# Kernel optimization log

Measured on AMD Instinct MI355X. Metric: run time of the kernel, lower is better.

## Reference

```python
import jax, jax.numpy as jnp
import numpy as np

B, T, D = 2, 2048, 1024
H = 16
HD = D // H
NE = 17  # n_edge_types + 1

def setup_inputs() -> dict:
    key = jax.random.key(0)
    ks = jax.random.split(key, 6)
    x = jax.random.normal(ks[0], (B, T, D), dtype=jnp.float32)
    graph_adj = jax.random.uniform(ks[1], (B, T, T), dtype=jnp.float32)
    edge_types = jax.random.randint(ks[2], (B, T, T), 0, NE, dtype=jnp.int32)
    Wqkv = jax.random.normal(ks[3], (D, 3 * D), dtype=jnp.float32) * (D ** -0.5)
    Wproj = jax.random.normal(ks[4], (D, D), dtype=jnp.float32) * (D ** -0.5)
    adj_bias = jnp.zeros((H,), dtype=jnp.float32)
    edge_table = jax.random.normal(ks[5], (NE, H), dtype=jnp.float32) * 0.02
    return {"x": x, "graph_adj": graph_adj, "edge_types": edge_types,
            "Wqkv": Wqkv, "Wproj": Wproj, "adj_bias": adj_bias,
            "edge_table": edge_table}

def reference(x, graph_adj, edge_types, Wqkv, Wproj, adj_bias, edge_table):
    Bc, Tc, C = x.shape
    qkv = (x @ Wqkv).reshape(Bc, Tc, 3, H, HD)
    q, k, v = qkv[:, :, 0], qkv[:, :, 1], qkv[:, :, 2]  # [B,T,H,HD]
    scale = 1.0 / jnp.sqrt(jnp.asarray(HD, dtype=x.dtype))
    # scores: [B,H,T,T]
    attn = jnp.einsum('bqhd,bkhd->bhqk', q, k) * scale
    # adjacency bias per head
    attn = attn + adj_bias[None, :, None, None] * graph_adj[:, None, :, :]
    # edge-type bias: lookup [B,T,T,H] -> [B,H,T,T]
    etype_b = edge_table[edge_types]  # [B,T,T,H]
    attn = attn + jnp.transpose(etype_b, (0, 3, 1, 2))
    # causal mask (upper triangle, diag=1)
    causal = jnp.triu(jnp.ones((Tc, Tc), dtype=bool), k=1)
    attn = jnp.where(causal[None, None, :, :], jnp.asarray(-jnp.inf, dtype=attn.dtype), attn)
    attn = jax.nn.softmax(attn, axis=-1)
    out = jnp.einsum('bhqk,bkhd->bqhd', attn, v).reshape(Bc, Tc, C)
    return out @ Wproj
```

## Files before the change

### kernel.cpp

```cpp
#include <hip/hip_runtime.h>
#include <stdint.h>

#define TT 2048
#define HH 16
#define LOG2E 1.44269504089f

typedef _Float16 f16;
typedef __attribute__((ext_vector_type(8))) _Float16 f16x8;
typedef __attribute__((ext_vector_type(4))) float f32x4;
typedef unsigned short ushort_t;

__device__ __forceinline__ void gl_lds16(const void* g, void* l){
  __builtin_amdgcn_global_load_lds(
      (__attribute__((address_space(1))) void*)(void*)g,
      (__attribute__((address_space(3))) void*)l, 16, 0, 0);
}

__device__ __forceinline__ void lds_barrier(){
  __asm__ volatile("s_waitcnt lgkmcnt(0)\n\ts_barrier" ::: "memory");
}

template<int CTRL>
__device__ __forceinline__ float dpp_mov(float x){
  int xi = __builtin_bit_cast(int, x);
  return __builtin_bit_cast(float,
      __builtin_amdgcn_update_dpp(xi, xi, CTRL, 0xF, 0xF, false));
}
__device__ __forceinline__ float row_red_max(float x){
  x = fmaxf(x, dpp_mov<0xB1>(x));
  x = fmaxf(x, dpp_mov<0x4E>(x));
  x = fmaxf(x, dpp_mov<0x124>(x));
  x = fmaxf(x, dpp_mov<0x128>(x));
  return x;
}
__device__ __forceinline__ float row_red_sum(float x){
  x += dpp_mov<0xB1>(x);
  x += dpp_mov<0x4E>(x);
  x += dpp_mov<0x124>(x);
  x += dpp_mov<0x128>(x);
  return x;
}

struct SchedT { unsigned short v[80]; };
static constexpr SchedT make_sched(){
  SchedT s{};
  int idx = 0;
  for (int size = 8; size >= 1; --size){
    for (int qt = 31; qt >= 8; --qt){
      int full = qt >> 3;
      int tail = (qt & 7) + 1;
      if (size == 8)
        for (int ci = 0; ci < full; ++ci)
          s.v[idx++] = (unsigned short)(qt | (ci << 8));
      if (tail == size)
        s.v[idx++] = (unsigned short)(qt | (full << 8));
    }
    s.v[idx++] = (unsigned short)(size - 1);
  }
  return s;
}
__constant__ SchedT SCHED = make_sched();

__device__ __forceinline__ int slot_base(int qt){
  return (qt < 16) ? 2 * (qt - 8)
       : (qt < 24) ? 16 + 3 * (qt - 16)
                   : 40 + 4 * (qt - 24);
}

__global__ __launch_bounds__(256) void cvt_f2h_kernel(const float4* __restrict__ in,
                                                      uint2* __restrict__ out, int n4){
  int i = blockIdx.x * 256 + threadIdx.x;
  if (i >= n4) return;
  float4 v = in[i];
  union { f16 h[4]; uint2 u; } o;
  o.h[0] = (f16)v.x; o.h[1] = (f16)v.y; o.h[2] = (f16)v.z; o.h[3] = (f16)v.w;
  out[i] = o.u;
}

__global__ __launch_bounds__(256) void pack_bias_kernel(const float* __restrict__ gadj,
                                                        const int* __restrict__ etype,
                                                        uint32_t* __restrict__ out){
  int bid = blockIdx.x;
  int b = bid / 528, ti = bid - b * 528;
  int qt = (int)((sqrtf(8.f * (float)ti + 1.f) - 1.f) * 0.5f);
  while ((qt + 1) * (qt + 2) / 2 <= ti) ++qt;
  while (qt * (qt + 1) / 2 > ti) --qt;
  int kt = ti - qt * (qt + 1) / 2;

  int t = threadIdx.x;
  int row = t >> 2, c0 = (t & 3) << 4;
  size_t src = ((size_t)b * TT + qt * 64 + row) * TT + kt * 64 + c0;
  uint32_t* dst = out + (size_t)bid * 4096;
  int wq = (row >> 4) * 64 + ((row & 15) >> 2) * 16;
  int jbase = (t & 3) * 4 + (row & 3);
  #pragma unroll
  for (int v4 = 0; v4 < 4; ++v4){
    float4 g = *(const float4*)(gadj + src + v4 * 4);
    int4   e = *(const int4*)(etype + src + v4 * 4);
    union { f16 h; ushort_t u; } c;
    c.h = (f16)g.x; dst[(wq + v4 * 4 + 0) * 16 + jbase] = (uint32_t)c.u | ((uint32_t)e.x << 16);
    c.h = (f16)g.y; dst[(wq + v4 * 4 + 1) * 16 + jbase] = (uint32_t)c.u | ((uint32_t)e.y << 16);
    c.h = (f16)g.z; dst[(wq + v4 * 4 + 2) * 16 + jbase] = (uint32_t)c.u | ((uint32_t)e.z << 16);
    c.h = (f16)g.w; dst[(wq + v4 * 4 + 3) * 16 + jbase] = (uint32_t)c.u | ((uint32_t)e.w << 16);
  }
}

__global__ __launch_bounds__(256) void transpose_cvt_kernel(const float* __restrict__ in,
                                                            f16* __restrict__ out, int R, int C){
  __shared__ float tile[64][65];
  int c0 = blockIdx.x * 64, r0 = blockIdx.y * 64;
  int t = threadIdx.x;
  int row = t >> 2, cs = (t & 3) << 4;
  const float4* src = (const float4*)(in + (size_t)(r0 + row) * C + c0 + cs);
  float4 a = src[0], b = src[1], c = src[2], d = src[3];
  float* tr = &tile[row][cs];
  tr[0]=a.x; tr[1]=a.y; tr[2]=a.z;  tr[3]=a.w;
  tr[4]=b.x; tr[5]=b.y; tr[6]=b.z;  tr[7]=b.w;
  tr[8]=c.x; tr[9]=c.y; tr[10]=c.z; tr[11]=c.w;
  tr[12]=d.x;tr[13]=d.y;tr[14]=d.z; tr[15]=d.w;
  __syncthreads();
  f16 tmp[16];
  #pragma unroll
  for (int j = 0; j < 16; ++j) tmp[j] = (f16)tile[cs + j][row];
  f16* dst = out + (size_t)(c0 + row) * R + r0 + cs;
  *(uint4*)dst = *(uint4*)&tmp[0];
  *(uint4*)(dst + 8) = *(uint4*)&tmp[8];
}

__global__ __launch_bounds__(256) void gemm_f16_kernel(const f16* __restrict__ A,
                                                       const f16* __restrict__ Bt,
                                                       void* __restrict__ Cout,
                                                       int M, int N, int K, int out_f32){
  __shared__ __align__(16) f16 As[128 * 32];
  __shared__ __align__(16) f16 Bs[128 * 32];
  int t = threadIdx.x;
  int w = t >> 6, lane = t & 63;
  int wm = (w >> 1) * 64, wn = (w & 1) * 64;
  int lrow = lane & 15, quad = lane >> 4;
  int bm = blockIdx.y, bn = blockIdx.x;

  f32x4 acc[4][4];
  for (int i = 0; i < 4; ++i)
    for (int j = 0; j < 4; ++j)
      for (int r = 0; r < 4; ++r) acc[i][j][r] = 0.f;

  const int nk = K >> 5;
  for (int kt = 0; kt < nk; ++kt){
    int k0 = kt << 5;
    __syncthreads();
    #pragma unroll
    for (int i = 0; i < 2; ++i){
      int c = (w << 7) + (i << 6) + lane;
      gl_lds16(A  + (size_t)((bm << 7) + (c >> 2)) * K + k0 + ((c & 3) << 3),
               As + ((w << 7) + (i << 6)) * 8);
      gl_lds16(Bt + (size_t)((bn << 7) + (c >> 2)) * K + k0 + ((c & 3) << 3),
               Bs + ((w << 7) + (i << 6)) * 8);
    }
    __syncthreads();
    f16x8 af[4], bfr[4];
    #pragma unroll
    for (int mi = 0; mi < 4; ++mi)
      af[mi] = *(const f16x8*)(As + (wm + mi * 16 + lrow) * 32 + quad * 8);
    #pragma unroll
    for (int ni = 0; ni < 4; ++ni)
      bfr[ni] = *(const f16x8*)(Bs + (wn + ni * 16 + lrow) * 32 + quad * 8);
    #pragma unroll
    for (int mi = 0; mi < 4; ++mi)
      #pragma unroll
      for (int ni = 0; ni < 4; ++ni)
        acc[mi][ni] = __builtin_amdgcn_mfma_f32_16x16x32_f16(af[mi], bfr[ni], acc[mi][ni], 0, 0, 0);
  }

  #pragma unroll
  for (int mi = 0; mi < 4; ++mi)
    #pragma unroll
    for (int ni = 0; ni < 4; ++ni)
      #pragma unroll
      for (int r = 0; r < 4; ++r){
        int row = (bm << 7) + wm + mi * 16 + quad * 4 + r;
        int col = (bn << 7) + wn + ni * 16 + lrow;
        float val = acc[mi][ni][r];
        if (out_f32) ((float*)Cout)[(size_t)row * N + col] = val;
        else         ((f16*)Cout)[(size_t)row * N + col] = (f16)val;
      }
}

__global__ __launch_bounds__(256, 4) void attn_kernel(const f16* __restrict__ qkv,
                                                      const uint32_t* __restrict__ pbias,
                                                      const float* __restrict__ adj_bias,
                                                      const float* __restrict__ edge_table,
                                                      f16* __restrict__ attn_out,
                                                      f16* __restrict__ Opart,
                                                      float* __restrict__ MLpart){
  __shared__ __align__(16) f16 Ks[64 * 72];
  __shared__ __align__(16) f16 Vt[64 * 72];
  __shared__ __align__(16) f16 Ps[4][16 * 72];
  __shared__ float edge_lds[32 * 17];

  int bx = blockIdx.x;
  int bh = bx & 31;
  int h = bh & 15, b = bh >> 4;
  int ej = SCHED.v[bx >> 5];
  int qt = ej & 31, ci = ej >> 8;
  int ksrt = ci << 3;
  int kend = min(qt, ksrt + 7);
  bool whole = (qt < 8);

  int t = threadIdx.x;
  int w = t >> 6, lane = t & 63;
  int lrow = lane & 15, quad = lane >> 4;

  for (int i = t; i < 544; i += 256)
    edge_lds[i] = edge_table[(i % 17) * HH + h] * LOG2E;
  float adjb = adj_bias[h] * LOG2E;
  int erep = (lane & 31) * 17;

  int q0 = qt * 64 + w * 16;
  const size_t qrow = ((size_t)b * TT + q0 + lrow) * 3072 + h * 64;
  f16x8 qf0 = *(const f16x8*)(qkv + qrow + quad * 8);
  f16x8 qf1 = *(const f16x8*)(qkv + qrow + 32 + quad * 8);

  f32x4 o[4];
  for (int i = 0; i < 4; ++i)
    for (int r = 0; r < 4; ++r) o[i][r] = 0.f;
  float mrun[4] = {-1e30f, -1e30f, -1e30f, -1e30f};
  float lrun[4] = {0.f, 0.f, 0.f, 0.f};

  const int keyA = (t >> 3) << 1;
  const int hdA  = (t & 7) << 3;
  const int sA   = ((keyA >> 3) ^ (hdA >> 3)) & 7;
  const f16* kbase = qkv + (size_t)b * TT * 3072 + 1024 + h * 64;
  const f16* vbase = qkv + (size_t)b * TT * 3072 + 2048 + h * 64;
  const size_t koffA = (size_t)keyA * 3072 + hdA;
  const size_t koffB = koffA + 3072;

  const float SCL = 0.125f * LOG2E;

  const int tribase = b * 528 + ((qt * (qt + 1)) >> 1);
  const uint32_t* bthread = pbias + ((size_t)t << 4);
  const int qgb = q0 + quad * 4;

  uint4 ka, kb, va, vb;
  {
    const f16* kr = kbase + (size_t)(ksrt * 64) * 3072;
    const f16* vr = vbase + (size_t)(ksrt * 64) * 3072;
    ka = *(const uint4*)(kr + koffA); kb = *(const uint4*)(kr + koffB);
    va = *(const uint4*)(vr + koffA); vb = *(const uint4*)(vr + koffB);
  }

  for (int kt2 = ksrt; kt2 <= kend; ++kt2){
    lds_barrier();
    union B4 { uint4 v; uint32_t e[4]; } bb0, bb1, bb2, bb3;
    {
      const uint32_t* tp = bthread + ((size_t)(tribase + kt2) << 12);
      bb0.v = *(const uint4*)(tp + 0);
      bb1.v = *(const uint4*)(tp + 4);
      bb2.v = *(const uint4*)(tp + 8);
      bb3.v = *(const uint4*)(tp + 12);
    }
    *(uint4*)(Ks + keyA * 72 + hdA) = ka;
    *(uint4*)(Ks + (keyA + 1) * 72 + hdA) = kb;
    {
      union { uint4 u; f16 hh[8]; } ua, ub;
      ua.u = va; ub.u = vb;
      #pragma unroll
      for (int jj = 0; jj < 8; ++jj){
        union { f16 h[2]; uint32_t wv; } pr;
        pr.h[0] = ua.hh[jj]; pr.h[1] = ub.hh[jj];
        *(uint32_t*)(Vt + (hdA + jj) * 72 + (sA << 3) + (keyA & 7)) = pr.wv;
      }
    }
    if (kt2 < kend){
      const f16* kr = kbase + (size_t)((kt2 + 1) * 64) * 3072;
      const f16* vr = vbase + (size_t)((kt2 + 1) * 64) * 3072;
      ka = *(const uint4*)(kr + koffA); kb = *(const uint4*)(kr + koffB);
      va = *(const uint4*)(vr + koffA); vb = *(const uint4*)(vr + koffB);
    }
    lds_barrier();

    f32x4 sf[4];
    #pragma unroll
    for (int nb = 0; nb < 4; ++nb){
      f32x4 s = {0.f, 0.f, 0.f, 0.f};
      f16x8 kf0 = *(const f16x8*)(Ks + (nb * 16 + lrow) * 72 + quad * 8);
      f16x8 kf1 = *(const f16x8*)(Ks + (nb * 16 + lrow) * 72 + 32 + quad * 8);
      s = __builtin_amdgcn_mfma_f32_16x16x32_f16(qf0, kf0, s, 0, 0, 0);
      s = __builtin_amdgcn_mfma_f32_16x16x32_f16(qf1, kf1, s, 0, 0, 0);
      sf[nb] = s;
    }

    int kgb = kt2 * 64 + lrow;
    float sarr[4][4];
    bool diag = (kt2 == qt);
#define MASK_NB(nb, BB)                                                          \
    {                                                                            \
      int kg = kgb + nb * 16;                                                    \
      _Pragma("unroll")                                                          \
      for (int r = 0; r < 4; ++r){                                               \
        float v;                                                                 \
        if (diag && kg > qgb + r) v = -1e30f;                                    \
        else {                                                                   \
          uint32_t bp = BB.e[r];                                                 \
          union { ushort_t u; f16 h; } cv; cv.u = (ushort_t)bp;                  \
          v = sf[nb][r] * SCL + adjb * (float)cv.h + edge_lds[erep + (bp >> 16)];\
        }                                                                        \
        sarr[nb][r] = v;                                                         \
      }                                                                          \
    }
    MASK_NB(0, bb0)
    MASK_NB(1, bb1)
    MASK_NB(2, bb2)
    MASK_NB(3, bb3)
#undef MASK_NB

    float mx[4];
    bool need = false;
    #pragma unroll
    for (int r = 0; r < 4; ++r){
      float m_ = fmaxf(fmaxf(sarr[0][r], sarr[1][r]), fmaxf(sarr[2][r], sarr[3][r]));
      m_ = row_red_max(m_);
      mx[r] = m_;
      need = need || (m_ > mrun[r] + 5.0f);
    }
    if (__any(need)){
      #pragma unroll
      for (int r = 0; r < 4; ++r){
        float mnew = fmaxf(mrun[r], mx[r]);
        float alpha = exp2f(mrun[r] - mnew);
        lrun[r] *= alpha;
        #pragma unroll
        for (int nbh = 0; nbh < 4; ++nbh) o[nbh][r] *= alpha;
        mrun[r] = mnew;
      }
    }
    float pv_[4][4];
    #pragma unroll
    for (int r = 0; r < 4; ++r){
      float rs = 0.f;
      #pragma unroll
      for (int nb = 0; nb < 4; ++nb){
        float p = exp2f(sarr[nb][r] - mrun[r]);
        pv_[nb][r] = p; rs += p;
      }
      rs = row_red_sum(rs);
      lrun[r] += rs;
    }

    f16* Pw = &Ps[w][0];
    #pragma unroll
    for (int nb = 0; nb < 4; ++nb)
      #pragma unroll
      for (int r = 0; r < 4; ++r)
        Pw[(quad * 4 + r) * 72 + nb * 16 + lrow] = (f16)pv_[nb][r];
    __asm__ volatile("s_waitcnt lgkmcnt(0)" ::: "memory");

    #pragma unroll
    for (int cc = 0; cc < 2; ++cc){
      f16x8 pf = *(const f16x8*)(Pw + lrow * 72 + cc * 32 + quad * 8);
      #pragma unroll
      for (int nbh = 0; nbh < 4; ++nbh){
        int hd = nbh * 16 + lrow;
        int sb = (hd >> 3) & 7;
        f16x8 vf = *(const f16x8*)(Vt + hd * 72 + (((cc * 4 + quad) ^ sb) << 3));
        o[nbh] = __builtin_amdgcn_mfma_f32_16x16x32_f16(pf, vf, o[nbh], 0, 0, 0);
      }
    }
  }

  if (whole){
    float inv[4];
    #pragma unroll
    for (int r = 0; r < 4; ++r) inv[r] = 1.0f / lrun[r];
    #pragma unroll
    for (int nbh = 0; nbh < 4; ++nbh)
      #pragma unroll
      for (int r = 0; r < 4; ++r){
        int qg = q0 + quad * 4 + r;
        int col = h * 64 + nbh * 16 + lrow;
        attn_out[((size_t)b * TT + qg) * 1024 + col] = (f16)(o[nbh][r] * inv[r]);
      }
  } else {
    int slot = bh * 72 + slot_base(qt) + ci;
    f16* Ob = Opart + (size_t)slot * 4096;
    #pragma unroll
    for (int nbh = 0; nbh < 4; ++nbh)
      #pragma unroll
      for (int r = 0; r < 4; ++r)
        Ob[(w * 16 + quad * 4 + r) * 64 + nbh * 16 + lrow] = (f16)o[nbh][r];
    if (lrow == 0){
      #pragma unroll
      for (int r = 0; r < 4; ++r){
        int qq = w * 16 + quad * 4 + r;
        MLpart[(size_t)slot * 128 + qq] = mrun[r];
        MLpart[(size_t)slot * 128 + 64 + qq] = lrun[r];
      }
    }
  }
}

__global__ __launch_bounds__(256) void combine_kernel(const f16* __restrict__ Opart,
                                                      const float* __restrict__ ML,
                                                      f16* __restrict__ attn_out){
  int qt = blockIdx.x + 8;
  int bh = blockIdx.y;
  int nch = (qt >> 3) + 1;
  int slot0 = bh * 72 + slot_base(qt);
  int t = threadIdx.x;
  int q = t >> 2;
  int hd0 = (t & 3) << 4;

  float m[4], l[4];
  float M = -1e30f;
  #pragma unroll
  for (int c = 0; c < 4; ++c){
    if (c < nch){
      m[c] = ML[(size_t)(slot0 + c) * 128 + q];
      l[c] = ML[(size_t)(slot0 + c) * 128 + 64 + q];
      M = fmaxf(M, m[c]);
    } else { m[c] = -1e30f; l[c] = 0.f; }
  }
  float acc[16];
  #pragma unroll
  for (int i = 0; i < 16; ++i) acc[i] = 0.f;
  float L = 0.f;
  #pragma unroll
  for (int c = 0; c < 4; ++c){
    if (c < nch){
      float wgt = exp2f(m[c] - M);
      L += l[c] * wgt;
      const f16* O = Opart + (size_t)(slot0 + c) * 4096 + q * 64 + hd0;
      f16x8 a0 = *(const f16x8*)O, a1 = *(const f16x8*)(O + 8);
      #pragma unroll
      for (int i = 0; i < 8; ++i){
        acc[i]     += (float)a0[i] * wgt;
        acc[i + 8] += (float)a1[i] * wgt;
      }
    }
  }
  float invL = 1.0f / L;
  f16 outv[16];
  #pragma unroll
  for (int i = 0; i < 16; ++i) outv[i] = (f16)(acc[i] * invL);
  int b = bh >> 4, h = bh & 15;
  f16* dst = attn_out + ((size_t)b * TT + qt * 64 + q) * 1024 + h * 64 + hd0;
  *(uint4*)dst = *(uint4*)&outv[0];
  *(uint4*)(dst + 8) = *(uint4*)&outv[8];
}

extern "C" void kernel_launch(void* const* d_in, const int* in_sizes, int n_in,
                              void* d_out, int out_size, void* d_ws, size_t ws_size,
                              hipStream_t stream){
  (void)in_sizes; (void)n_in; (void)out_size; (void)ws_size;
  const float* x_f32  = (const float*)d_in[0];
  const float* gadj   = (const float*)d_in[1];
  const int*   etype  = (const int*)d_in[2];
  const float* wqkv   = (const float*)d_in[3];
  const float* wproj  = (const float*)d_in[4];
  const float* adjb   = (const float*)d_in[5];
  const float* etab   = (const float*)d_in[6];

  char* ws = (char*)d_ws;
  f16*     x_f16  = (f16*)(ws);
  f16*     qkv    = (f16*)(ws + (8u  << 20));
  f16*     wqkvT  = (f16*)(ws + (32u << 20));
  f16*     Opart  = (f16*)(ws + (32u << 20));
  f16*     wprojT = (f16*)(ws + (51u << 20));
  float*   MLpart = (float*)(ws + (53u << 20));
  uint32_t* pbias = (uint32_t*)(ws + (55u << 20));
  f16*     attn_o = x_f16;

  cvt_f2h_kernel<<<4096, 256, 0, stream>>>((const float4*)x_f32, (uint2*)x_f16, 1048576);
  pack_bias_kernel<<<1056, 256, 0, stream>>>(gadj, etype, pbias);
  transpose_cvt_kernel<<<dim3(48, 16), 256, 0, stream>>>(wqkv, wqkvT, 1024, 3072);
  transpose_cvt_kernel<<<dim3(16, 16), 256, 0, stream>>>(wproj, wprojT, 1024, 1024);
  gemm_f16_kernel<<<dim3(24, 32), 256, 0, stream>>>(x_f16, wqkvT, qkv, 4096, 3072, 1024, 0);
  attn_kernel<<<2560, 256, 0, stream>>>(qkv, pbias, adjb, etab, attn_o, Opart, MLpart);
  combine_kernel<<<dim3(24, 32), 256, 0, stream>>>(Opart, MLpart, attn_o);
  gemm_f16_kernel<<<dim3(8, 32), 256, 0, stream>>>(attn_o, wprojT, d_out, 4096, 1024, 1024, 1);
}
```

Before: 282.9 us.

## Process two query tiles per attention block to reuse loaded K/V tiles

```diff
diff --git a/kernel.cpp b/kernel.cpp
--- a/kernel.cpp
+++ b/kernel.cpp
@@ -41,30 +41,25 @@
   return x;
 }
 
-struct SchedT { unsigned short v[80]; };
+struct SchedT { unsigned short v[40]; };
 static constexpr SchedT make_sched(){
-  SchedT s{};
-  int idx = 0;
-  for (int size = 8; size >= 1; --size){
-    for (int qt = 31; qt >= 8; --qt){
-      int full = qt >> 3;
-      int tail = (qt & 7) + 1;
+  SchedT s{}; int idx = 0;
+  for (int size = 8; size >= 1; --size)
+    for (int J = 15; J >= 0; --J){
+      int NT = 2 * J + 2;
+      int f = NT >> 3, tail = NT - (f << 3);
       if (size == 8)
-        for (int ci = 0; ci < full; ++ci)
-          s.v[idx++] = (unsigned short)(qt | (ci << 8));
-      if (tail == size)
-        s.v[idx++] = (unsigned short)(qt | (full << 8));
-    }
-    s.v[idx++] = (unsigned short)(size - 1);
-  }
+        for (int ci = 0; ci < f; ++ci) s.v[idx++] = (unsigned short)(J | (ci << 4));
+      if (tail == size) s.v[idx++] = (unsigned short)(J | (f << 4));
+    }
   return s;
 }
 __constant__ SchedT SCHED = make_sched();
 
-__device__ __forceinline__ int slot_base(int qt){
-  return (qt < 16) ? 2 * (qt - 8)
-       : (qt < 24) ? 16 + 3 * (qt - 16)
-                   : 40 + 4 * (qt - 24);
+__device__ __forceinline__ int slot_base(int J){
+  return (J < 8) ? 2 * (J - 4)
+       : (J < 12) ? 8 + 3 * (J - 8)
+                  : 20 + 4 * (J - 12);
 }
 
 __global__ __launch_bounds__(256) void cvt_f2h_kernel(const float4* __restrict__ in,
@@ -185,7 +180,7 @@
       }
 }
 
-__global__ __launch_bounds__(256, 4) void attn_kernel(const f16* __restrict__ qkv,
+__global__ __launch_bounds__(256, 3) void attn_kernel(const f16* __restrict__ qkv,
                                                       const uint32_t* __restrict__ pbias,
                                                       const float* __restrict__ adj_bias,
                                                       const float* __restrict__ edge_table,
@@ -194,17 +189,18 @@
                                                       float* __restrict__ MLpart){
   __shared__ __align__(16) f16 Ks[64 * 72];
   __shared__ __align__(16) f16 Vt[64 * 72];
-  __shared__ __align__(16) f16 Ps[4][16 * 72];
+  __shared__ __align__(16) f16 Ps[4][2][16 * 72];
   __shared__ float edge_lds[32 * 17];
 
   int bx = blockIdx.x;
   int bh = bx & 31;
   int h = bh & 15, b = bh >> 4;
-  int ej = SCHED.v[bx >> 5];
-  int qt = ej & 31, ci = ej >> 8;
-  int ksrt = ci << 3;
-  int kend = min(qt, ksrt + 7);
-  bool whole = (qt < 8);
+  int e = SCHED.v[bx >> 5];
+  int J = e & 15, ci = e >> 4;
+  int kts = ci << 3;
+  int kte = min(2 * J + 1, kts + 7);
+  bool whole = (J <= 3);
+  int qtA = 2 * J, qtB = 2 * J + 1;
 
   int t = threadIdx.x;
   int w = t >> 6, lane = t & 63;
@@ -215,16 +211,20 @@
   float adjb = adj_bias[h] * LOG2E;
   int erep = (lane & 31) * 17;
 
-  int q0 = qt * 64 + w * 16;
-  const size_t qrow = ((size_t)b * TT + q0 + lrow) * 3072 + h * 64;
-  f16x8 qf0 = *(const f16x8*)(qkv + qrow + quad * 8);
-  f16x8 qf1 = *(const f16x8*)(qkv + qrow + 32 + quad * 8);
-
-  f32x4 o[4];
+  int qa0 = J * 128 + w * 16;
+  int qb0 = qa0 + 64;
+  const size_t qrowA = ((size_t)b * TT + qa0 + lrow) * 3072 + h * 64;
+  const size_t qrowB = ((size_t)b * TT + qb0 + lrow) * 3072 + h * 64;
+  f16x8 qfa0 = *(const f16x8*)(qkv + qrowA + quad * 8);
+  f16x8 qfa1 = *(const f16x8*)(qkv + qrowA + 32 + quad * 8);
+  f16x8 qfb0 = *(const f16x8*)(qkv + qrowB + quad * 8);
+  f16x8 qfb1 = *(const f16x8*)(qkv + qrowB + 32 + quad * 8);
+
+  f32x4 oa[4], ob[4];
   for (int i = 0; i < 4; ++i)
-    for (int r = 0; r < 4; ++r) o[i][r] = 0.f;
-  float mrun[4] = {-1e30f, -1e30f, -1e30f, -1e30f};
-  float lrun[4] = {0.f, 0.f, 0.f, 0.f};
+    for (int r = 0; r < 4; ++r){ oa[i][r] = 0.f; ob[i][r] = 0.f; }
+  float mra[4] = {-1e30f,-1e30f,-1e30f,-1e30f}, mrb[4] = {-1e30f,-1e30f,-1e30f,-1e30f};
+  float lra[4] = {0.f,0.f,0.f,0.f},             lrb[4] = {0.f,0.f,0.f,0.f};
 
   const int keyA = (t >> 3) << 1;
   const int hdA  = (t & 7) << 3;
@@ -236,27 +236,33 @@
 
   const float SCL = 0.125f * LOG2E;
 
-  const int tribase = b * 528 + ((qt * (qt + 1)) >> 1);
-  const uint32_t* bthread = pbias + ((size_t)t << 4);
-  const int qgb = q0 + quad * 4;
+  const int triA = b * 528 + ((qtA * (qtA + 1)) >> 1);
+  const int triB = b * 528 + ((qtB * (qtB + 1)) >> 1);
+  const uint32_t* bthr = pbias + ((size_t)t << 4);
+  const int qgbA = qa0 + quad * 4;
+  const int qgbB = qb0 + quad * 4;
 
   uint4 ka, kb, va, vb;
   {
-    const f16* kr = kbase + (size_t)(ksrt * 64) * 3072;
-    const f16* vr = vbase + (size_t)(ksrt * 64) * 3072;
+    const f16* kr = kbase + (size_t)(kts * 64) * 3072;
+    const f16* vr = vbase + (size_t)(kts * 64) * 3072;
     ka = *(const uint4*)(kr + koffA); kb = *(const uint4*)(kr + koffB);
     va = *(const uint4*)(vr + koffA); vb = *(const uint4*)(vr + koffB);
   }
 
-  for (int kt2 = ksrt; kt2 <= kend; ++kt2){
+  for (int kt2 = kts; kt2 <= kte; ++kt2){
+    bool act_a = (kt2 <= qtA);
     lds_barrier();
-    union B4 { uint4 v; uint32_t e[4]; } bb0, bb1, bb2, bb3;
+    union B4 { uint4 v; uint32_t e[4]; } a0, a1, a2, a3, c0, c1, c2, c3;
+    if (act_a){
+      const uint32_t* tp = bthr + ((size_t)(triA + kt2) << 12);
+      a0.v = *(const uint4*)(tp + 0);  a1.v = *(const uint4*)(tp + 4);
+      a2.v = *(const uint4*)(tp + 8);  a3.v = *(const uint4*)(tp + 12);
+    }
     {
-      const uint32_t* tp = bthread + ((size_t)(tribase + kt2) << 12);
-      bb0.v = *(const uint4*)(tp + 0);
-      bb1.v = *(const uint4*)(tp + 4);
-      bb2.v = *(const uint4*)(tp + 8);
-      bb3.v = *(const uint4*)(tp + 12);
+      const uint32_t* tp = bthr + ((size_t)(triB + kt2) << 12);
+      c0.v = *(const uint4*)(tp + 0);  c1.v = *(const uint4*)(tp + 4);
+      c2.v = *(const uint4*)(tp + 8);  c3.v = *(const uint4*)(tp + 12);
     }
     *(uint4*)(Ks + keyA * 72 + hdA) = ka;
     *(uint4*)(Ks + (keyA + 1) * 72 + hdA) = kb;
@@ -270,7 +276,7 @@
         *(uint32_t*)(Vt + (hdA + jj) * 72 + (sA << 3) + (keyA & 7)) = pr.wv;
       }
     }
-    if (kt2 < kend){
+    if (kt2 < kte){
       const f16* kr = kbase + (size_t)((kt2 + 1) * 64) * 3072;
       const f16* vr = vbase + (size_t)((kt2 + 1) * 64) * 3072;
       ka = *(const uint4*)(kr + koffA); kb = *(const uint4*)(kr + koffB);
@@ -278,121 +284,161 @@
     }
     lds_barrier();
 
-    f32x4 sf[4];
+    f32x4 sa[4], sbv[4];
     #pragma unroll
     for (int nb = 0; nb < 4; ++nb){
-      f32x4 s = {0.f, 0.f, 0.f, 0.f};
       f16x8 kf0 = *(const f16x8*)(Ks + (nb * 16 + lrow) * 72 + quad * 8);
       f16x8 kf1 = *(const f16x8*)(Ks + (nb * 16 + lrow) * 72 + 32 + quad * 8);
-      s = __builtin_amdgcn_mfma_f32_16x16x32_f16(qf0, kf0, s, 0, 0, 0);
-      s = __builtin_amdgcn_mfma_f32_16x16x32_f16(qf1, kf1, s, 0, 0, 0);
-      sf[nb] = s;
+      f32x4 s = {0.f, 0.f, 0.f, 0.f};
+      if (act_a){
+        s = __builtin_amdgcn_mfma_f32_16x16x32_f16(qfa0, kf0, s, 0, 0, 0);
+        s = __builtin_amdgcn_mfma_f32_16x16x32_f16(qfa1, kf1, s, 0, 0, 0);
+      }
+      sa[nb] = s;
+      f32x4 s2 = {0.f, 0.f, 0.f, 0.f};
+      s2 = __builtin_amdgcn_mfma_f32_16x16x32_f16(qfb0, kf0, s2, 0, 0, 0);
+      s2 = __builtin_amdgcn_mfma_f32_16x16x32_f16(qfb1, kf1, s2, 0, 0, 0);
+      sbv[nb] = s2;
     }
 
     int kgb = kt2 * 64 + lrow;
-    float sarr[4][4];
-    bool diag = (kt2 == qt);
-#define MASK_NB(nb, BB)                                                          \
+
+#define MASK_NB(SARR, SF, nb, BB, DIAG, QGB)                                     \
     {                                                                            \
       int kg = kgb + nb * 16;                                                    \
       _Pragma("unroll")                                                          \
       for (int r = 0; r < 4; ++r){                                               \
         float v;                                                                 \
-        if (diag && kg > qgb + r) v = -1e30f;                                    \
+        if (DIAG && kg > QGB + r) v = -1e30f;                                    \
         else {                                                                   \
           uint32_t bp = BB.e[r];                                                 \
           union { ushort_t u; f16 h; } cv; cv.u = (ushort_t)bp;                  \
-          v = sf[nb][r] * SCL + adjb * (float)cv.h + edge_lds[erep + (bp >> 16)];\
+          v = SF[nb][r] * SCL + adjb * (float)cv.h + edge_lds[erep + (bp >> 16)];\
         }                                                                        \
-        sarr[nb][r] = v;                                                         \
+        SARR[nb][r] = v;                                                         \
       }                                                                          \
     }
-    MASK_NB(0, bb0)
-    MASK_NB(1, bb1)
-    MASK_NB(2, bb2)
-    MASK_NB(3, bb3)
+
+#define SOFTMAX_SUB(SARR, MR, LR, OO, PV)                                        \
+    {                                                                            \
+      float mx[4]; bool need = false;                                            \
+      _Pragma("unroll")                                                          \
+      for (int r = 0; r < 4; ++r){                                               \
+        float m_ = fmaxf(fmaxf(SARR[0][r], SARR[1][r]),                          \
+                         fmaxf(SARR[2][r], SARR[3][r]));                         \
+        m_ = row_red_max(m_);                                                    \
+        mx[r] = m_;                                                              \
+        need = need || (m_ > MR[r] + 5.0f);                                      \
+      }                                                                          \
+      if (__any(need)){                                                          \
+        _Pragma("unroll")                                                        \
+        for (int r = 0; r < 4; ++r){                                             \
+          float mnew = fmaxf(MR[r], mx[r]);                                      \
+          float alpha = exp2f(MR[r] - mnew);                                     \
+          LR[r] *= alpha;                                                        \
+          _Pragma("unroll")                                                      \
+          for (int nbh = 0; nbh < 4; ++nbh) OO[nbh][r] *= alpha;                 \
+          MR[r] = mnew;                                                          \
+        }                                                                        \
+      }                                                                          \
+      _Pragma("unroll")                                                          \
+      for (int r = 0; r < 4; ++r){                                               \
+        float rs = 0.f;                                                          \
+        _Pragma("unroll")                                                        \
+        for (int nb = 0; nb < 4; ++nb){                                          \
+          float p = exp2f(SARR[nb][r] - MR[r]);                                  \
+          PV[nb][r] = p; rs += p;                                                \
+        }                                                                        \
+        rs = row_red_sum(rs);                                                    \
+        LR[r] += rs;                                                             \
+      }                                                                          \
+    }
+
+    float pva[4][4], pvb[4][4];
+    if (act_a){
+      bool diagA = (kt2 == qtA);
+      float sarr[4][4];
+      MASK_NB(sarr, sa, 0, a0, diagA, qgbA)
+      MASK_NB(sarr, sa, 1, a1, diagA, qgbA)
+      MASK_NB(sarr, sa, 2, a2, diagA, qgbA)
+      MASK_NB(sarr, sa, 3, a3, diagA, qgbA)
+      SOFTMAX_SUB(sarr, mra, lra, oa, pva)
+      f16* Pw = &Ps[w][0][0];
+      #pragma unroll
+      for (int nb = 0; nb < 4; ++nb)
+        #pragma unroll
+        for (int r = 0; r < 4; ++r)
+          Pw[(quad * 4 + r) * 72 + nb * 16 + lrow] = (f16)pva[nb][r];
+    }
+    {
+      bool diagB = (kt2 == qtB);
+      float sarr[4][4];
+      MASK_NB(sarr, sbv, 0, c0, diagB, qgbB)
+      MASK_NB(sarr, sbv, 1, c1, diagB, qgbB)
+      MASK_NB(sarr, sbv, 2, c2, diagB, qgbB)
+      MASK_NB(sarr, sbv, 3, c3, diagB, qgbB)
+      SOFTMAX_SUB(sarr, mrb, lrb, ob, pvb)
+      f16* Pw = &Ps[w][1][0];
+      #pragma unroll
+      for (int nb = 0; nb < 4; ++nb)
+        #pragma unroll
+        for (int r = 0; r < 4; ++r)
+          Pw[(quad * 4 + r) * 72 + nb * 16 + lrow] = (f16)pvb[nb][r];
+    }
 #undef MASK_NB
-
-    float mx[4];
-    bool need = false;
-    #pragma unroll
-    for (int r = 0; r < 4; ++r){
-      float m_ = fmaxf(fmaxf(sarr[0][r], sarr[1][r]), fmaxf(sarr[2][r], sarr[3][r]));
-      m_ = row_red_max(m_);
-      mx[r] = m_;
-      need = need || (m_ > mrun[r] + 5.0f);
-    }
-    if (__any(need)){
-      #pragma unroll
-      for (int r = 0; r < 4; ++r){
-        float mnew = fmaxf(mrun[r], mx[r]);
-        float alpha = exp2f(mrun[r] - mnew);
-        lrun[r] *= alpha;
-        #pragma unroll
-        for (int nbh = 0; nbh < 4; ++nbh) o[nbh][r] *= alpha;
-        mrun[r] = mnew;
-      }
-    }
-    float pv_[4][4];
-    #pragma unroll
-    for (int r = 0; r < 4; ++r){
-      float rs = 0.f;
-      #pragma unroll
-      for (int nb = 0; nb < 4; ++nb){
-        float p = exp2f(sarr[nb][r] - mrun[r]);
-        pv_[nb][r] = p; rs += p;
-      }
-      rs = row_red_sum(rs);
-      lrun[r] += rs;
-    }
-
-    f16* Pw = &Ps[w][0];
-    #pragma unroll
-    for (int nb = 0; nb < 4; ++nb)
-      #pragma unroll
-      for (int r = 0; r < 4; ++r)
-        Pw[(quad * 4 + r) * 72 + nb * 16 + lrow] = (f16)pv_[nb][r];
+#undef SOFTMAX_SUB
     __asm__ volatile("s_waitcnt lgkmcnt(0)" ::: "memory");
 
     #pragma unroll
     for (int cc = 0; cc < 2; ++cc){
-      f16x8 pf = *(const f16x8*)(Pw + lrow * 72 + cc * 32 + quad * 8);
+      f16x8 pfa = {};
+      if (act_a) pfa = *(const f16x8*)(&Ps[w][0][0] + lrow * 72 + cc * 32 + quad * 8);
+      f16x8 pfb = *(const f16x8*)(&Ps[w][1][0] + lrow * 72 + cc * 32 + quad * 8);
       #pragma unroll
       for (int nbh = 0; nbh < 4; ++nbh){
         int hd = nbh * 16 + lrow;
         int sb = (hd >> 3) & 7;
         f16x8 vf = *(const f16x8*)(Vt + hd * 72 + (((cc * 4 + quad) ^ sb) << 3));
-        o[nbh] = __builtin_amdgcn_mfma_f32_16x16x32_f16(pf, vf, o[nbh], 0, 0, 0);
+        if (act_a) oa[nbh] = __builtin_amdgcn_mfma_f32_16x16x32_f16(pfa, vf, oa[nbh], 0, 0, 0);
+        ob[nbh] = __builtin_amdgcn_mfma_f32_16x16x32_f16(pfb, vf, ob[nbh], 0, 0, 0);
       }
     }
   }
 
   if (whole){
-    float inv[4];
-    #pragma unroll
-    for (int r = 0; r < 4; ++r) inv[r] = 1.0f / lrun[r];
+    float inva[4], invb[4];
+    #pragma unroll
+    for (int r = 0; r < 4; ++r){ inva[r] = 1.0f / lra[r]; invb[r] = 1.0f / lrb[r]; }
     #pragma unroll
     for (int nbh = 0; nbh < 4; ++nbh)
       #pragma unroll
       for (int r = 0; r < 4; ++r){
-        int qg = q0 + quad * 4 + r;
         int col = h * 64 + nbh * 16 + lrow;
-        attn_out[((size_t)b * TT + qg) * 1024 + col] = (f16)(o[nbh][r] * inv[r]);
+        int qga = qa0 + quad * 4 + r;
+        attn_out[((size_t)b * TT + qga) * 1024 + col] = (f16)(oa[nbh][r] * inva[r]);
+        int qgb2 = qb0 + quad * 4 + r;
+        attn_out[((size_t)b * TT + qgb2) * 1024 + col] = (f16)(ob[nbh][r] * invb[r]);
       }
   } else {
-    int slot = bh * 72 + slot_base(qt) + ci;
-    f16* Ob = Opart + (size_t)slot * 4096;
+    int slot = bh * 36 + slot_base(J) + ci;
+    f16* Ob = Opart + (size_t)slot * 8192;
     #pragma unroll
     for (int nbh = 0; nbh < 4; ++nbh)
       #pragma unroll
-      for (int r = 0; r < 4; ++r)
-        Ob[(w * 16 + quad * 4 + r) * 64 + nbh * 16 + lrow] = (f16)o[nbh][r];
+      for (int r = 0; r < 4; ++r){
+        int col = nbh * 16 + lrow;
+        int rowa = w * 16 + quad * 4 + r;
+        Ob[rowa * 64 + col] = (f16)oa[nbh][r];
+        Ob[(64 + rowa) * 64 + col] = (f16)ob[nbh][r];
+      }
     if (lrow == 0){
       #pragma unroll
       for (int r = 0; r < 4; ++r){
         int qq = w * 16 + quad * 4 + r;
-        MLpart[(size_t)slot * 128 + qq] = mrun[r];
-        MLpart[(size_t)slot * 128 + 64 + qq] = lrun[r];
+        MLpart[(size_t)slot * 256 + qq] = mra[r];
+        MLpart[(size_t)slot * 256 + 128 + qq] = lra[r];
+        MLpart[(size_t)slot * 256 + 64 + qq] = mrb[r];
+        MLpart[(size_t)slot * 256 + 128 + 64 + qq] = lrb[r];
       }
     }
   }
@@ -401,50 +447,56 @@
 __global__ __launch_bounds__(256) void combine_kernel(const f16* __restrict__ Opart,
                                                       const float* __restrict__ ML,
                                                       f16* __restrict__ attn_out){
-  int qt = blockIdx.x + 8;
+  int J = blockIdx.x + 4;
   int bh = blockIdx.y;
-  int nch = (qt >> 3) + 1;
-  int slot0 = bh * 72 + slot_base(qt);
+  int nch = (J < 8) ? 2 : ((J < 12) ? 3 : 4);
+  int slot0 = bh * 36 + slot_base(J);
   int t = threadIdx.x;
-  int q = t >> 2;
-  int hd0 = (t & 3) << 4;
+  int row = t >> 1;
+  int hd0 = (t & 1) << 5;
 
   float m[4], l[4];
   float M = -1e30f;
   #pragma unroll
   for (int c = 0; c < 4; ++c){
     if (c < nch){
-      m[c] = ML[(size_t)(slot0 + c) * 128 + q];
-      l[c] = ML[(size_t)(slot0 + c) * 128 + 64 + q];
+      m[c] = ML[(size_t)(slot0 + c) * 256 + row];
+      l[c] = ML[(size_t)(slot0 + c) * 256 + 128 + row];
       M = fmaxf(M, m[c]);
     } else { m[c] = -1e30f; l[c] = 0.f; }
   }
-  float acc[16];
-  #pragma unroll
-  for (int i = 0; i < 16; ++i) acc[i] = 0.f;
+  float acc[32];
+  #pragma unroll
+  for (int i = 0; i < 32; ++i) acc[i] = 0.f;
   float L = 0.f;
   #pragma unroll
   for (int c = 0; c < 4; ++c){
     if (c < nch){
       float wgt = exp2f(m[c] - M);
       L += l[c] * wgt;
-      const f16* O = Opart + (size_t)(slot0 + c) * 4096 + q * 64 + hd0;
-      f16x8 a0 = *(const f16x8*)O, a1 = *(const f16x8*)(O + 8);
+      const f16* O = Opart + (size_t)(slot0 + c) * 8192 + row * 64 + hd0;
+      f16x8 a0 = *(const f16x8*)O,        a1 = *(const f16x8*)(O + 8);
+      f16x8 a2 = *(const f16x8*)(O + 16), a3 = *(const f16x8*)(O + 24);
       #pragma unroll
       for (int i = 0; i < 8; ++i){
-        acc[i]     += (float)a0[i] * wgt;
-        acc[i + 8] += (float)a1[i] * wgt;
+        acc[i]      += (float)a0[i] * wgt;
+        acc[i + 8]  += (float)a1[i] * wgt;
+        acc[i + 16] += (float)a2[i] * wgt;
+        acc[i + 24] += (float)a3[i] * wgt;
       }
     }
   }
   float invL = 1.0f / L;
-  f16 outv[16];
-  #pragma unroll
-  for (int i = 0; i < 16; ++i) outv[i] = (f16)(acc[i] * invL);
+  f16 outv[32];
+  #pragma unroll
+  for (int i = 0; i < 32; ++i) outv[i] = (f16)(acc[i] * invL);
   int b = bh >> 4, h = bh & 15;
-  f16* dst = attn_out + ((size_t)b * TT + qt * 64 + q) * 1024 + h * 64 + hd0;
+  int qg = J * 128 + row;
+  f16* dst = attn_out + ((size_t)b * TT + qg) * 1024 + h * 64 + hd0;
   *(uint4*)dst = *(uint4*)&outv[0];
   *(uint4*)(dst + 8) = *(uint4*)&outv[8];
+  *(uint4*)(dst + 16) = *(uint4*)&outv[16];
+  *(uint4*)(dst + 24) = *(uint4*)&outv[24];
 }
 
 extern "C" void kernel_launch(void* const* d_in, const int* in_sizes, int n_in,
@@ -474,7 +526,7 @@
   transpose_cvt_kernel<<<dim3(48, 16), 256, 0, stream>>>(wqkv, wqkvT, 1024, 3072);
   transpose_cvt_kernel<<<dim3(16, 16), 256, 0, stream>>>(wproj, wprojT, 1024, 1024);
   gemm_f16_kernel<<<dim3(24, 32), 256, 0, stream>>>(x_f16, wqkvT, qkv, 4096, 3072, 1024, 0);
-  attn_kernel<<<2560, 256, 0, stream>>>(qkv, pbias, adjb, etab, attn_o, Opart, MLpart);
-  combine_kernel<<<dim3(24, 32), 256, 0, stream>>>(Opart, MLpart, attn_o);
+  attn_kernel<<<1280, 256, 0, stream>>>(qkv, pbias, adjb, etab, attn_o, Opart, MLpart);
+  combine_kernel<<<dim3(12, 32), 256, 0, stream>>>(Opart, MLpart, attn_o);
   gemm_f16_kernel<<<dim3(8, 32), 256, 0, stream>>>(attn_o, wprojT, d_out, 4096, 1024, 1024, 1);
 }
```

Measured after the change: 557.9 us. 1.97x slower.
